# Performance work log

Hardware: AMD Instinct MI355X
Metric: run time of the kernel (lower is better)

Reference implementation:

```python
import jax, jax.numpy as jnp
import numpy as np

PATCH = 3      # forward default patch_size
ALPHA = 1.0    # forward default alpha
# scale_factor = 1 -> F.interpolate is the identity


def setup_inputs() -> dict:
    key = jax.random.key(0)
    x_l = jax.random.normal(key, (16, 1, 1536, 1536), dtype=jnp.float32)
    return {"x_l": x_l}


def reference(x_l):
    # x_l: [N, 1, H, W]
    N, C, H, W = x_l.shape
    p = PATCH
    pad = p // 2
    # zero-padded input, matching F.unfold's implicit zero padding
    xp = jnp.pad(x_l, ((0, 0), (0, 0), (pad, pad), (pad, pad)))
    # gather the p*p shifted views -> [N, p*p, H, W] (equivalent to F.unfold for C=1;
    # softmax + weighted sum over dim 1 is permutation-invariant over the patch axis)
    local = jnp.stack(
        [xp[:, 0, i:i + H, j:j + W] for i in range(p) for j in range(p)],
        axis=1,
    )
    # local_difference = local_l - x_l**2  (broadcast over the patch dim)
    diff = local - x_l[:, 0][:, None, :, :] ** 2
    corr = jax.nn.softmax(-diff / ALPHA, axis=1)
    # softmax-weighted local average -> [N, 1, H, W]
    return jnp.sum(corr * local, axis=1, keepdims=True)
```

## Files before the change

### kernel.cpp

```cpp
#include <hip/hip_runtime.h>
#include <math.h>

#define IMG_W 1536
#define IMG_H 1536
#define NIMG  16

typedef float f32x4 __attribute__((ext_vector_type(4)));

__global__ __launch_bounds__(128, 8)
void WeightedAverage_55551107006568_kernel(const float* __restrict__ x,
                                           float* __restrict__ out) {
    const int tid = threadIdx.x;
    const int w0  = ((blockIdx.x << 7) + tid) << 2;
    const int h   = blockIdx.y;
    const size_t plane = (size_t)blockIdx.z * ((size_t)IMG_H * IMG_W);
    const float* xp = x + plane + w0;
    float* op = out + plane;

    const bool lok = (w0 > 0);
    const bool rok = (w0 + 4 < IMG_W);
    const int offL = lok ? -4 : 0;
    const int offR = rok ? 16 : 0;

    const bool tv = (h > 0);
    const bool bv = (h < IMG_H - 1);
    const int hm = tv ? h - 1 : 0;
    const int hp = bv ? h + 1 : IMG_H - 1;

    const float* r0 = xp + (size_t)hm * IMG_W;
    const float* r1 = xp + (size_t)h  * IMG_W;
    const float* r2 = xp + (size_t)hp * IMG_W;

    f32x4 m0 = *(const f32x4*)r0;
    float a0 = *(const float*)((const char*)r0 + offL);
    float b0 = *(const float*)((const char*)r0 + offR);
    f32x4 m1 = *(const f32x4*)r1;
    float a1 = *(const float*)((const char*)r1 + offL);
    float b1 = *(const float*)((const char*)r1 + offR);
    f32x4 m2 = *(const f32x4*)r2;
    float a2 = *(const float*)((const char*)r2 + offL);
    float b2 = *(const float*)((const char*)r2 + offR);
    __builtin_amdgcn_sched_barrier(0);

    if (!tv) { m0 = (f32x4){0.f, 0.f, 0.f, 0.f}; a0 = 0.f; b0 = 0.f; }
    if (!bv) { m2 = (f32x4){0.f, 0.f, 0.f, 0.f}; a2 = 0.f; b2 = 0.f; }
    if (!lok) { a0 = 0.f; a1 = 0.f; a2 = 0.f; }
    if (!rok) { b0 = 0.f; b1 = 0.f; b2 = 0.f; }

    f32x4 den = {0.f, 0.f, 0.f, 0.f};
    f32x4 num = {0.f, 0.f, 0.f, 0.f};
    {
        const f32x4 mr[3] = {m0, m1, m2};
        const float ha[3] = {a0, a1, a2};
        const float hb[3] = {b0, b1, b2};
#pragma unroll
        for (int i = 0; i < 3; ++i) {
            const f32x4 mm = mr[i];
            const float eL = __expf(-ha[i]), vL = ha[i] * eL;
            const float e0 = __expf(-mm.x),  v0 = mm.x * e0;
            const float e1 = __expf(-mm.y),  v1 = mm.y * e1;
            const float e2 = __expf(-mm.z),  v2 = mm.z * e2;
            const float e3 = __expf(-mm.w),  v3 = mm.w * e3;
            const float eR = __expf(-hb[i]), vR = hb[i] * eR;
            den.x += eL + e0 + e1;  num.x += vL + v0 + v1;
            den.y += e0 + e1 + e2;  num.y += v0 + v1 + v2;
            den.z += e1 + e2 + e3;  num.z += v1 + v2 + v3;
            den.w += e2 + e3 + eR;  num.w += v2 + v3 + vR;
        }
    }

    f32x4 o;
    o.x = __fdividef(num.x, den.x);
    o.y = __fdividef(num.y, den.y);
    o.z = __fdividef(num.z, den.z);
    o.w = __fdividef(num.w, den.w);
    __builtin_nontemporal_store(o, (f32x4*)(op + (size_t)h * IMG_W + w0));
}

extern "C" void kernel_launch(void* const* d_in, const int* in_sizes, int n_in,
                              void* d_out, int out_size, void* d_ws, size_t ws_size,
                              hipStream_t stream) {
    const float* x = (const float*)d_in[0];
    float* out = (float*)d_out;
    dim3 grid(IMG_W / (128 * 4), IMG_H, NIMG);
    dim3 block(128, 1, 1);
    WeightedAverage_55551107006568_kernel<<<grid, block, 0, stream>>>(x, out);
}
```

Baseline: 267.8 us.

## Compute two rows per thread and swizzle blocks so each XCD owns whole images

Each thread now produces two vertically adjacent output rows from four loaded input rows, so the horizontal exp sums of the two shared middle rows are computed once. The grid is flattened to 1D and remapped so that blocks on the same XCD (bid&7) cover the same pair of images, which keeps neighbouring-row reloads in that XCD's L2. The trade-off is more registers per thread and half as many blocks.

```diff
diff --git a/kernel.cpp b/kernel.cpp
--- a/kernel.cpp
+++ b/kernel.cpp
@@ -4,57 +4,68 @@
 #define IMG_W 1536
 #define IMG_H 1536
 #define NIMG  16
+#define RPB   2
 
 typedef float f32x4 __attribute__((ext_vector_type(4)));
 
 __global__ __launch_bounds__(128, 8)
 void WeightedAverage_55551107006568_kernel(const float* __restrict__ x,
                                            float* __restrict__ out) {
-    const int tid = threadIdx.x;
-    const int w0  = ((blockIdx.x << 7) + tid) << 2;
-    const int h   = blockIdx.y;
-    const size_t plane = (size_t)blockIdx.z * ((size_t)IMG_H * IMG_W);
+    const int bid   = blockIdx.x;
+    const int xcd   = bid & 7;
+    const int chunk = bid >> 3;
+    const int z     = (xcd << 1) + (chunk / 2304);
+    const int rem   = chunk % 2304;
+    const int yb    = rem / 3;
+    const int xb    = rem - yb * 3;
+    const int h0    = yb << 1;
+    const int w0    = ((xb << 7) + threadIdx.x) << 2;
+
+    const size_t plane = (size_t)z * ((size_t)IMG_H * IMG_W);
     const float* xp = x + plane + w0;
-    float* op = out + plane;
+    float* op = out + plane + w0;
 
     const bool lok = (w0 > 0);
     const bool rok = (w0 + 4 < IMG_W);
     const int offL = lok ? -4 : 0;
     const int offR = rok ? 16 : 0;
 
-    const bool tv = (h > 0);
-    const bool bv = (h < IMG_H - 1);
-    const int hm = tv ? h - 1 : 0;
-    const int hp = bv ? h + 1 : IMG_H - 1;
+    const bool tv = (h0 > 0);
+    const bool bv = (h0 + 2 < IMG_H);
+    const int rt = tv ? h0 - 1 : 0;
+    const int rb = bv ? h0 + 2 : IMG_H - 1;
 
-    const float* r0 = xp + (size_t)hm * IMG_W;
-    const float* r1 = xp + (size_t)h  * IMG_W;
-    const float* r2 = xp + (size_t)hp * IMG_W;
+    const float* rp0 = xp + (size_t)rt * IMG_W;
+    const float* rp1 = xp + (size_t)h0 * IMG_W;
+    const float* rp2 = xp + (size_t)(h0 + 1) * IMG_W;
+    const float* rp3 = xp + (size_t)rb * IMG_W;
 
-    f32x4 m0 = *(const f32x4*)r0;
-    float a0 = *(const float*)((const char*)r0 + offL);
-    float b0 = *(const float*)((const char*)r0 + offR);
-    f32x4 m1 = *(const f32x4*)r1;
-    float a1 = *(const float*)((const char*)r1 + offL);
-    float b1 = *(const float*)((const char*)r1 + offR);
-    f32x4 m2 = *(const f32x4*)r2;
-    float a2 = *(const float*)((const char*)r2 + offL);
-    float b2 = *(const float*)((const char*)r2 + offR);
+    f32x4 m0 = *(const f32x4*)rp0;
+    float a0 = *(const float*)((const char*)rp0 + offL);
+    float b0 = *(const float*)((const char*)rp0 + offR);
+    f32x4 m1 = *(const f32x4*)rp1;
+    float a1 = *(const float*)((const char*)rp1 + offL);
+    float b1 = *(const float*)((const char*)rp1 + offR);
+    f32x4 m2 = *(const f32x4*)rp2;
+    float a2 = *(const float*)((const char*)rp2 + offL);
+    float b2 = *(const float*)((const char*)rp2 + offR);
+    f32x4 m3 = *(const f32x4*)rp3;
+    float a3 = *(const float*)((const char*)rp3 + offL);
+    float b3 = *(const float*)((const char*)rp3 + offR);
     __builtin_amdgcn_sched_barrier(0);
 
     if (!tv) { m0 = (f32x4){0.f, 0.f, 0.f, 0.f}; a0 = 0.f; b0 = 0.f; }
-    if (!bv) { m2 = (f32x4){0.f, 0.f, 0.f, 0.f}; a2 = 0.f; b2 = 0.f; }
-    if (!lok) { a0 = 0.f; a1 = 0.f; a2 = 0.f; }
-    if (!rok) { b0 = 0.f; b1 = 0.f; b2 = 0.f; }
+    if (!bv) { m3 = (f32x4){0.f, 0.f, 0.f, 0.f}; a3 = 0.f; b3 = 0.f; }
+    if (!lok) { a0 = 0.f; a1 = 0.f; a2 = 0.f; a3 = 0.f; }
+    if (!rok) { b0 = 0.f; b1 = 0.f; b2 = 0.f; b3 = 0.f; }
 
-    f32x4 den = {0.f, 0.f, 0.f, 0.f};
-    f32x4 num = {0.f, 0.f, 0.f, 0.f};
+    f32x4 he[4], hv[4];
     {
-        const f32x4 mr[3] = {m0, m1, m2};
-        const float ha[3] = {a0, a1, a2};
-        const float hb[3] = {b0, b1, b2};
+        const f32x4 mr[4] = {m0, m1, m2, m3};
+        const float ha[4] = {a0, a1, a2, a3};
+        const float hb[4] = {b0, b1, b2, b3};
 #pragma unroll
-        for (int i = 0; i < 3; ++i) {
+        for (int i = 0; i < 4; ++i) {
             const f32x4 mm = mr[i];
             const float eL = __expf(-ha[i]), vL = ha[i] * eL;
             const float e0 = __expf(-mm.x),  v0 = mm.x * e0;
@@ -62,19 +73,24 @@
             const float e2 = __expf(-mm.z),  v2 = mm.z * e2;
             const float e3 = __expf(-mm.w),  v3 = mm.w * e3;
             const float eR = __expf(-hb[i]), vR = hb[i] * eR;
-            den.x += eL + e0 + e1;  num.x += vL + v0 + v1;
-            den.y += e0 + e1 + e2;  num.y += v0 + v1 + v2;
-            den.z += e1 + e2 + e3;  num.z += v1 + v2 + v3;
-            den.w += e2 + e3 + eR;  num.w += v2 + v3 + vR;
+            he[i] = (f32x4){eL + e0 + e1, e0 + e1 + e2, e1 + e2 + e3, e2 + e3 + eR};
+            hv[i] = (f32x4){vL + v0 + v1, v0 + v1 + v2, v1 + v2 + v3, v2 + v3 + vR};
         }
     }
 
-    f32x4 o;
-    o.x = __fdividef(num.x, den.x);
-    o.y = __fdividef(num.y, den.y);
-    o.z = __fdividef(num.z, den.z);
-    o.w = __fdividef(num.w, den.w);
-    __builtin_nontemporal_store(o, (f32x4*)(op + (size_t)h * IMG_W + w0));
+    const f32x4 ce = he[1] + he[2];
+    const f32x4 cv = hv[1] + hv[2];
+    const f32x4 den0 = ce + he[0], num0 = cv + hv[0];
+    const f32x4 den1 = ce + he[3], num1 = cv + hv[3];
+
+    f32x4 o0, o1;
+#pragma unroll
+    for (int p = 0; p < 4; ++p) {
+        o0[p] = __fdividef(num0[p], den0[p]);
+        o1[p] = __fdividef(num1[p], den1[p]);
+    }
+    __builtin_nontemporal_store(o0, (f32x4*)(op + (size_t)h0 * IMG_W));
+    __builtin_nontemporal_store(o1, (f32x4*)(op + (size_t)(h0 + 1) * IMG_W));
 }
 
 extern "C" void kernel_launch(void* const* d_in, const int* in_sizes, int n_in,
@@ -82,7 +98,7 @@
                               hipStream_t stream) {
     const float* x = (const float*)d_in[0];
     float* out = (float*)d_out;
-    dim3 grid(IMG_W / (128 * 4), IMG_H, NIMG);
+    dim3 grid(36864, 1, 1);
     dim3 block(128, 1, 1);
     WeightedAverage_55551107006568_kernel<<<grid, block, 0, stream>>>(x, out);
 }
```

After: 259.6 us. 1.03x faster.
